# Kernel optimization log

Hardware: AMD Instinct MI355X
Metric: run time of the kernel (lower is better)

Reference implementation:

```python
import jax, jax.numpy as jnp
import numpy as np

B, T, C = 8, 2048, 1024
E, K = 8, 2
CF = 1.0
LB_W = 0.01
H = 4 * C
N = B * T
CAP = max(int(N * K / E * CF), 1)  # 4096
NEG_INF = -1e30


def setup_inputs() -> dict:
    key = jax.random.key(0)
    ks = jax.random.split(key, 10)
    s_r = (2.0 / (C + E)) ** 0.5  # xavier_normal for router linears
    s1 = 1.0 / np.sqrt(C)
    s2 = 1.0 / np.sqrt(H)
    return {
        "x": jax.random.normal(ks[0], (B, T, C), jnp.float32),
        "noise": jax.random.normal(ks[1], (B, T, E), jnp.float32),
        "w_route": jax.random.normal(ks[2], (E, C), jnp.float32) * s_r,
        "b_route": jnp.zeros((E,), jnp.float32),
        "w_noise": jax.random.normal(ks[3], (E, C), jnp.float32) * s_r,
        "b_noise": jnp.zeros((E,), jnp.float32),
        "w1": jax.random.uniform(ks[4], (E, C, H), jnp.float32, -s1, s1),
        "b1": jax.random.uniform(ks[5], (E, H), jnp.float32, -s1, s1),
        "w2": jax.random.uniform(ks[6], (E, H, C), jnp.float32, -s2, s2),
        "b2": jax.random.uniform(ks[7], (E, C), jnp.float32, -s2, s2),
    }


def reference(x, noise, w_route, b_route, w_noise, b_noise, w1, b1, w2, b2):
    # ---- NoisyTopkRouter ----
    logits = jnp.einsum('btc,ec->bte', x, w_route) + b_route          # (B,T,E)
    noise_std = jax.nn.softplus(jnp.einsum('btc,ec->bte', x, w_noise) + b_noise)
    noisy = logits + noise * noise_std
    topk_vals, topk_idx = jax.lax.top_k(noisy, K)                     # (B,T,K)
    # sparse softmax: -inf everywhere except top-k slots
    onehot = jax.nn.one_hot(topk_idx, E, dtype=noisy.dtype)           # (B,T,K,E)
    sel = onehot.max(axis=-2) > 0                                     # (B,T,E) bool
    gates = jax.nn.softmax(jnp.where(sel, noisy, NEG_INF), axis=-1)   # (B,T,E)

    # ---- load balancing loss ----
    frac = gates.mean(axis=(0, 1))
    lb_loss = jnp.mean((frac - 1.0 / E) ** 2)

    # ---- capacity-limited dispatch (faithful: first-come order, cap per expert) ----
    gates_f = gates.reshape(N, E)
    mask_f = sel.reshape(N, E)
    pos = jnp.cumsum(mask_f.astype(jnp.int32), axis=0) - 1            # rank within expert
    keep = mask_f & (pos < CAP)
    tok = jnp.broadcast_to(jnp.arange(N, dtype=jnp.int32)[:, None], (N, E))
    eid = jnp.broadcast_to(jnp.arange(E, dtype=jnp.int32)[None, :], (N, E))
    slot = jnp.where(keep, pos, CAP)                                  # CAP = out of bounds -> dropped
    dispatch = jnp.full((E, CAP), N, dtype=jnp.int32)
    dispatch = dispatch.at[eid.ravel(), slot.ravel()].set(tok.ravel(), mode='drop')

    # ---- gather -> per-expert MLP -> weighted scatter ----
    x_pad = jnp.concatenate([x.reshape(N, C), jnp.zeros((1, C), x.dtype)], axis=0)
    xe = x_pad[dispatch]                                              # (E,CAP,C)
    h = jax.nn.relu(jnp.einsum('etc,ech->eth', xe, w1) + b1[:, None, :])
    ye = jnp.einsum('eth,ehc->etc', h, w2) + b2[:, None, :]           # (E,CAP,C)
    g_pad = jnp.concatenate([gates_f, jnp.zeros((1, E), gates_f.dtype)], axis=0)
    g = g_pad[dispatch, jnp.arange(E, dtype=jnp.int32)[:, None]]      # (E,CAP)
    weighted = ye * g[..., None]

    out = jnp.zeros((N + 1, C), x.dtype).at[dispatch.ravel()].add(
        weighted.reshape(E * CAP, C))[:N].reshape(B, T, C)
    return out, LB_W * lb_loss
```

## Files before the change

kernel.cpp:

```cpp
#include <hip/hip_runtime.h>

#define N_TOK 16384
#define C_DIM 1024
#define E_NUM 8
#define H_DIM 4096
#define CAPACITY 4096
#define LB_W 0.01f

typedef __bf16 bf16;
typedef bf16 bf16x8 __attribute__((ext_vector_type(8)));
typedef bf16 bf16x4 __attribute__((ext_vector_type(4)));
typedef float f32x4 __attribute__((ext_vector_type(4)));

__device__ __forceinline__ void gld_lds16(const void* g, void* l) {
  __builtin_amdgcn_global_load_lds((const __attribute__((address_space(1))) void*)g,
                                   (__attribute__((address_space(3))) void*)l,
                                   16, 0, 0);
}

__global__ void route_kernel(const float* __restrict__ x,
                             const float* __restrict__ noise,
                             const float* __restrict__ w_route,
                             const float* __restrict__ b_route,
                             const float* __restrict__ w_noise,
                             const float* __restrict__ b_noise,
                             float* __restrict__ gates,
                             int* __restrict__ maskT) {
  const int lane = threadIdx.x;
  const int n = blockIdx.x * blockDim.y + threadIdx.y;
  float xv[16];
#pragma unroll
  for (int i = 0; i < 16; ++i) xv[i] = x[(size_t)n * C_DIM + lane + 64 * i];
  float lr[E_NUM], ln[E_NUM];
#pragma unroll
  for (int e = 0; e < E_NUM; ++e) {
    float sr = 0.f, sn = 0.f;
#pragma unroll
    for (int i = 0; i < 16; ++i) {
      sr += xv[i] * w_route[e * C_DIM + lane + 64 * i];
      sn += xv[i] * w_noise[e * C_DIM + lane + 64 * i];
    }
#pragma unroll
    for (int off = 32; off; off >>= 1) {
      sr += __shfl_xor(sr, off, 64);
      sn += __shfl_xor(sn, off, 64);
    }
    lr[e] = sr;
    ln[e] = sn;
  }
  if (lane == 0) {
    float noisy[E_NUM];
#pragma unroll
    for (int e = 0; e < E_NUM; ++e) {
      float z = ln[e] + b_noise[e];
      float sp = fmaxf(z, 0.f) + log1pf(expf(-fabsf(z)));
      noisy[e] = lr[e] + b_route[e] + noise[n * E_NUM + e] * sp;
    }
    int i1 = 0;
    float v1 = noisy[0];
#pragma unroll
    for (int e = 1; e < E_NUM; ++e)
      if (noisy[e] > v1) { v1 = noisy[e]; i1 = e; }
    int i2 = -1;
    float v2 = -3.0e38f;
#pragma unroll
    for (int e = 0; e < E_NUM; ++e)
      if (e != i1 && noisy[e] > v2) { v2 = noisy[e]; i2 = e; }
    float e2 = expf(v2 - v1);
    float denom = 1.f + e2;
#pragma unroll
    for (int e = 0; e < E_NUM; ++e) {
      float g = (e == i1) ? (1.f / denom) : ((e == i2) ? (e2 / denom) : 0.f);
      gates[n * E_NUM + e] = g;
      maskT[(size_t)e * N_TOK + n] = (e == i1 || e == i2) ? 1 : 0;
    }
  }
}

__global__ __launch_bounds__(1024) void scan_kernel(
    const int* __restrict__ maskT, const float* __restrict__ gates,
    int* __restrict__ tok, float* __restrict__ gslot) {
  const int e = blockIdx.x;
  const int t = threadIdx.x;
  const int lane = t & 63, w = t >> 6;
  __shared__ int wt[16];

  int4 mv[4];
#pragma unroll
  for (int i = 0; i < 4; ++i)
    mv[i] = *(const int4*)(maskT + (size_t)e * N_TOK + t * 16 + i * 4);
  const int* m = (const int*)mv;
  int s = 0;
#pragma unroll
  for (int i = 0; i < 16; ++i) s += m[i];

  int v = s;
#pragma unroll
  for (int off = 1; off < 64; off <<= 1) {
    int u = __shfl_up(v, off, 64);
    if (lane >= off) v += u;
  }
  if (lane == 63) wt[w] = v;
  __syncthreads();
  int woff = 0;
#pragma unroll
  for (int i = 0; i < 16; ++i)
    if (i < w) woff += wt[i];

  int pos = woff + v - s;
#pragma unroll
  for (int i = 0; i < 16; ++i) {
    if (m[i] && pos < CAPACITY) {
      int n = t * 16 + i;
      tok[e * CAPACITY + pos] = n;
      gslot[e * CAPACITY + pos] = gates[n * E_NUM + e];
    }
    pos += m[i];
  }
}

__global__ void frac_kernel(const float* __restrict__ gates,
                            float* __restrict__ fracsum) {
  __shared__ float sm[E_NUM];
  int t = threadIdx.x;
  if (t < E_NUM) sm[t] = 0.f;
  __syncthreads();
  int g0 = blockIdx.x * 256 + t;
  float p = 0.f;
#pragma unroll
  for (int i = 0; i < (N_TOK * E_NUM) / (256 * 64); ++i)
    p += gates[g0 + i * 256 * 64];
  atomicAdd(&sm[t & 7], p);
  __syncthreads();
  if (t < E_NUM) atomicAdd(&fracsum[t], sm[t]);
}

__global__ void lb_kernel(const float* __restrict__ fracsum,
                          float* __restrict__ out_scalar) {
  if (threadIdx.x == 0) {
    float s = 0.f;
#pragma unroll
    for (int e = 0; e < E_NUM; ++e) {
      float f = fracsum[e] / (float)N_TOK - 0.125f;
      s += f * f;
    }
    out_scalar[0] = LB_W * (s / (float)E_NUM);
  }
}

__global__ void transpose_cvt(const float* __restrict__ src,
                              bf16* __restrict__ dst, int R, int S) {
  __shared__ float tile[32][33];
  const int e = blockIdx.z;
  const int r0 = blockIdx.y * 32;
  const int s0 = blockIdx.x * 32;
  const int t = threadIdx.x;
  const int rr = t >> 3, cc = (t & 7) * 4;
  const float4 v = *(const float4*)(src + ((size_t)e * R + (r0 + rr)) * S + s0 + cc);
  tile[rr][cc + 0] = v.x;
  tile[rr][cc + 1] = v.y;
  tile[rr][cc + 2] = v.z;
  tile[rr][cc + 3] = v.w;
  __syncthreads();
  bf16x4 o;
#pragma unroll
  for (int i = 0; i < 4; ++i) o[i] = (bf16)tile[cc + i][rr];
  *(bf16x4*)(dst + ((size_t)e * S + (s0 + rr)) * R + r0 + cc) = o;
}

__global__ void gather_xe(const float* __restrict__ x,
                          const int* __restrict__ tok, bf16* __restrict__ xe) {
  const int row = blockIdx.x;
  const int t = tok[row];
  const int c = threadIdx.x * 8;
  bf16x8 v;
  if (t >= 0) {
    const float4* xp = (const float4*)(x + (size_t)t * C_DIM + c);
    float4 a = xp[0], b = xp[1];
    v[0] = (bf16)a.x; v[1] = (bf16)a.y; v[2] = (bf16)a.z; v[3] = (bf16)a.w;
    v[4] = (bf16)b.x; v[5] = (bf16)b.y; v[6] = (bf16)b.z; v[7] = (bf16)b.w;
  } else {
#pragma unroll
    for (int i = 0; i < 8; ++i) v[i] = (bf16)0.f;
  }
  *(bf16x8*)(xe + (size_t)row * C_DIM + c) = v;
}

template <int EPI>
__global__ __launch_bounds__(256) void gemm_bt(
    const bf16* __restrict__ A0, size_t aStride, const bf16* __restrict__ B0,
    size_t bStride, int Kk, int Nn, const float* __restrict__ bias0,
    int biasStride, bf16* __restrict__ Hout0, size_t hStride,
    const int* __restrict__ tok0, const float* __restrict__ gslot0,
    float* __restrict__ Out) {
  const int z = blockIdx.z;
  const bf16* A = A0 + (size_t)z * aStride;
  const bf16* B = B0 + (size_t)z * bStride;
  const float* bias = bias0 + (size_t)z * biasStride;

  __shared__ bf16 As[128 * 32];
  __shared__ bf16 Bs[128 * 32];
  const int t = threadIdx.x;
  const int lane = t & 63;
  const int w = t >> 6;
  const int wm = (w >> 1) * 64;
  const int wn = (w & 1) * 64;
  const int bm = blockIdx.y * 128;
  const int bn = blockIdx.x * 128;

  f32x4 acc[4][4] = {};

  const int rowA = t >> 2;
  const int partA = (t & 3) << 4;
  const char* aP1 = (const char*)(A + (size_t)(bm + rowA) * Kk) + partA;
  const char* aP2 = (const char*)(A + (size_t)(bm + 64 + rowA) * Kk) + partA;
  const char* bP1 = (const char*)(B + (size_t)(bn + rowA) * Kk) + partA;
  const char* bP2 = (const char*)(B + (size_t)(bn + 64 + rowA) * Kk) + partA;
  char* asD1 = (char*)As + (t & 192) * 16;
  char* asD2 = (char*)As + 4096 + (t & 192) * 16;
  char* bsD1 = (char*)Bs + (t & 192) * 16;
  char* bsD2 = (char*)Bs + 4096 + (t & 192) * 16;

  for (int kt = 0; kt < Kk; kt += 32) {
    gld_lds16(aP1 + kt * 2, asD1);
    gld_lds16(aP2 + kt * 2, asD2);
    gld_lds16(bP1 + kt * 2, bsD1);
    gld_lds16(bP2 + kt * 2, bsD2);
    __syncthreads();
    bf16x8 af[4], bfr[4];
#pragma unroll
    for (int i = 0; i < 4; ++i) {
      af[i] = *(const bf16x8*)(As + (wm + i * 16 + (lane & 15)) * 32 + (lane >> 4) * 8);
      bfr[i] = *(const bf16x8*)(Bs + (wn + i * 16 + (lane & 15)) * 32 + (lane >> 4) * 8);
    }
#pragma unroll
    for (int i = 0; i < 4; ++i)
#pragma unroll
      for (int j = 0; j < 4; ++j)
        acc[i][j] = __builtin_amdgcn_mfma_f32_16x16x32_bf16(af[i], bfr[j], acc[i][j], 0, 0, 0);
    __syncthreads();
  }

  if (EPI == 0) {
    bf16* Hout = Hout0 + (size_t)z * hStride;
#pragma unroll
    for (int i = 0; i < 4; ++i) {
      const int rbase = bm + wm + i * 16 + (lane >> 4) * 4;
#pragma unroll
      for (int j = 0; j < 4; ++j) {
        const int col = bn + wn + j * 16 + (lane & 15);
        const float b = bias[col];
#pragma unroll
        for (int r = 0; r < 4; ++r) {
          float v = acc[i][j][r] + b;
          Hout[(size_t)(rbase + r) * Nn + col] = (bf16)fmaxf(v, 0.f);
        }
      }
    }
  } else {
    const int* tok = tok0 + (size_t)z * CAPACITY;
    const float* gslot = gslot0 + (size_t)z * CAPACITY;
#pragma unroll
    for (int i = 0; i < 4; ++i) {
      const int rbase = bm + wm + i * 16 + (lane >> 4) * 4;
#pragma unroll
      for (int r = 0; r < 4; ++r) {
        const int row = rbase + r;
        const int tk = tok[row];
        if (tk >= 0) {
          const float g = gslot[row];
#pragma unroll
          for (int j = 0; j < 4; ++j) {
            const int col = bn + wn + j * 16 + (lane & 15);
            atomicAdd(Out + (size_t)tk * C_DIM + col, g * (acc[i][j][r] + bias[col]));
          }
        }
      }
    }
  }
}

extern "C" void kernel_launch(void* const* d_in, const int* in_sizes, int n_in,
                              void* d_out, int out_size, void* d_ws,
                              size_t ws_size, hipStream_t stream) {
  const float* x = (const float*)d_in[0];
  const float* noise = (const float*)d_in[1];
  const float* w_route = (const float*)d_in[2];
  const float* b_route = (const float*)d_in[3];
  const float* w_noise = (const float*)d_in[4];
  const float* b_noise = (const float*)d_in[5];
  const float* w1 = (const float*)d_in[6];
  const float* b1 = (const float*)d_in[7];
  const float* w2 = (const float*)d_in[8];
  const float* b2 = (const float*)d_in[9];
  float* out = (float*)d_out;

  char* ws = (char*)d_ws;
  size_t off = 0;
  auto alloc = [&](size_t bytes) {
    char* p = ws + off;
    off += (bytes + 255) & ~(size_t)255;
    return p;
  };
  float* gates = (float*)alloc((size_t)N_TOK * E_NUM * 4);
  int* maskT = (int*)alloc((size_t)N_TOK * E_NUM * 4);
  int* tok = (int*)alloc((size_t)E_NUM * CAPACITY * 4);
  float* gslot = (float*)alloc((size_t)E_NUM * CAPACITY * 4);
  float* fracsum = (float*)alloc(256);
  bf16* xe = (bf16*)alloc((size_t)E_NUM * CAPACITY * C_DIM * 2);
  bf16* w1t = (bf16*)alloc((size_t)E_NUM * H_DIM * C_DIM * 2);
  bf16* w2t = (bf16*)alloc((size_t)E_NUM * C_DIM * H_DIM * 2);

  const size_t hPer = (size_t)CAPACITY * H_DIM * 2;
  size_t hAvail = (ws_size > off) ? (ws_size - off) : 0;
  int G = (int)(hAvail / hPer);
  if (G > E_NUM) G = E_NUM;
  if (G < 1) return;
  while (E_NUM % G) --G;
  bf16* hbuf = (bf16*)alloc((size_t)G * hPer);

  hipMemsetAsync(d_out, 0, (size_t)out_size * 4, stream);
  hipMemsetAsync(tok, 0xFF, (size_t)E_NUM * CAPACITY * 4, stream);
  hipMemsetAsync(fracsum, 0, 256, stream);

  transpose_cvt<<<dim3(H_DIM / 32, C_DIM / 32, E_NUM), 256, 0, stream>>>(w1, w1t, C_DIM, H_DIM);
  transpose_cvt<<<dim3(C_DIM / 32, H_DIM / 32, E_NUM), 256, 0, stream>>>(w2, w2t, H_DIM, C_DIM);

  route_kernel<<<dim3(N_TOK / 4), dim3(64, 4), 0, stream>>>(
      x, noise, w_route, b_route, w_noise, b_noise, gates, maskT);
  scan_kernel<<<E_NUM, 1024, 0, stream>>>(maskT, gates, tok, gslot);
  frac_kernel<<<64, 256, 0, stream>>>(gates, fracsum);
  lb_kernel<<<1, 64, 0, stream>>>(fracsum, out + (size_t)N_TOK * C_DIM);

  gather_xe<<<E_NUM * CAPACITY, 128, 0, stream>>>(x, tok, xe);

  for (int e0 = 0; e0 < E_NUM; e0 += G) {
    gemm_bt<0><<<dim3(H_DIM / 128, CAPACITY / 128, G), 256, 0, stream>>>(
        xe + (size_t)e0 * CAPACITY * C_DIM, (size_t)CAPACITY * C_DIM,
        w1t + (size_t)e0 * H_DIM * C_DIM, (size_t)H_DIM * C_DIM,
        C_DIM, H_DIM, b1 + (size_t)e0 * H_DIM, H_DIM,
        hbuf, (size_t)CAPACITY * H_DIM, nullptr, nullptr, nullptr);
    gemm_bt<1><<<dim3(C_DIM / 128, CAPACITY / 128, G), 256, 0, stream>>>(
        hbuf, (size_t)CAPACITY * H_DIM,
        w2t + (size_t)e0 * C_DIM * H_DIM, (size_t)C_DIM * H_DIM,
        H_DIM, C_DIM, b2 + (size_t)e0 * C_DIM, C_DIM,
        nullptr, 0, tok + (size_t)e0 * CAPACITY, gslot + (size_t)e0 * CAPACITY, out);
  }
}
```

Baseline: 1.499 ms.

## Merge gates and mask into transposed buffer; remap GEMM block order across XCDs

```diff
diff --git a/kernel.cpp b/kernel.cpp
--- a/kernel.cpp
+++ b/kernel.cpp
@@ -24,8 +24,7 @@
                              const float* __restrict__ b_route,
                              const float* __restrict__ w_noise,
                              const float* __restrict__ b_noise,
-                             float* __restrict__ gates,
-                             int* __restrict__ maskT) {
+                             float* __restrict__ gatesT) {
   const int lane = threadIdx.x;
   const int n = blockIdx.x * blockDim.y + threadIdx.y;
   float xv[16];
@@ -70,29 +69,32 @@
     float denom = 1.f + e2;
 #pragma unroll
     for (int e = 0; e < E_NUM; ++e) {
-      float g = (e == i1) ? (1.f / denom) : ((e == i2) ? (e2 / denom) : 0.f);
-      gates[n * E_NUM + e] = g;
-      maskT[(size_t)e * N_TOK + n] = (e == i1 || e == i2) ? 1 : 0;
+      float g = (e == i1) ? (1.f / denom) : ((e == i2) ? (e2 / denom) : -1.f);
+      gatesT[(size_t)e * N_TOK + n] = g;
     }
   }
 }
 
 __global__ __launch_bounds__(1024) void scan_kernel(
-    const int* __restrict__ maskT, const float* __restrict__ gates,
-    int* __restrict__ tok, float* __restrict__ gslot) {
+    const float* __restrict__ gatesT, int* __restrict__ tok,
+    float* __restrict__ gslot) {
   const int e = blockIdx.x;
   const int t = threadIdx.x;
   const int lane = t & 63, w = t >> 6;
   __shared__ int wt[16];
 
-  int4 mv[4];
+  float4 gv[4];
 #pragma unroll
   for (int i = 0; i < 4; ++i)
-    mv[i] = *(const int4*)(maskT + (size_t)e * N_TOK + t * 16 + i * 4);
-  const int* m = (const int*)mv;
+    gv[i] = *(const float4*)(gatesT + (size_t)e * N_TOK + t * 16 + i * 4);
+  const float* g = (const float*)gv;
+  int m[16];
   int s = 0;
 #pragma unroll
-  for (int i = 0; i < 16; ++i) s += m[i];
+  for (int i = 0; i < 16; ++i) {
+    m[i] = (g[i] >= 0.f) ? 1 : 0;
+    s += m[i];
+  }
 
   int v = s;
 #pragma unroll
@@ -111,28 +113,30 @@
 #pragma unroll
   for (int i = 0; i < 16; ++i) {
     if (m[i] && pos < CAPACITY) {
-      int n = t * 16 + i;
-      tok[e * CAPACITY + pos] = n;
-      gslot[e * CAPACITY + pos] = gates[n * E_NUM + e];
+      tok[e * CAPACITY + pos] = t * 16 + i;
+      gslot[e * CAPACITY + pos] = g[i];
     }
     pos += m[i];
   }
 }
 
-__global__ void frac_kernel(const float* __restrict__ gates,
+__global__ void frac_kernel(const float* __restrict__ gatesT,
                             float* __restrict__ fracsum) {
-  __shared__ float sm[E_NUM];
-  int t = threadIdx.x;
-  if (t < E_NUM) sm[t] = 0.f;
+  __shared__ float red[256];
+  const int e = blockIdx.x, t = threadIdx.x;
+  float s = 0.f;
+#pragma unroll
+  for (int i = 0; i < 16; ++i) {
+    float4 v = *(const float4*)(gatesT + (size_t)e * N_TOK + (i * 256 + t) * 4);
+    s += fmaxf(v.x, 0.f) + fmaxf(v.y, 0.f) + fmaxf(v.z, 0.f) + fmaxf(v.w, 0.f);
+  }
+  red[t] = s;
   __syncthreads();
-  int g0 = blockIdx.x * 256 + t;
-  float p = 0.f;
-#pragma unroll
-  for (int i = 0; i < (N_TOK * E_NUM) / (256 * 64); ++i)
-    p += gates[g0 + i * 256 * 64];
-  atomicAdd(&sm[t & 7], p);
-  __syncthreads();
-  if (t < E_NUM) atomicAdd(&fracsum[t], sm[t]);
+  for (int off = 128; off; off >>= 1) {
+    if (t < off) red[t] += red[t + off];
+    __syncthreads();
+  }
+  if (t == 0) fracsum[e] = red[0];
 }
 
 __global__ void lb_kernel(const float* __restrict__ fracsum,
@@ -198,6 +202,12 @@
   const bf16* B = B0 + (size_t)z * bStride;
   const float* bias = bias0 + (size_t)z * biasStride;
 
+  const int nbid = blockIdx.y * gridDim.x + blockIdx.x;
+  const int per = (gridDim.x * gridDim.y) >> 3;
+  const int lin = (nbid & 7) * per + (nbid >> 3);
+  const int bm = (lin / gridDim.x) * 128;
+  const int bn = (lin % gridDim.x) * 128;
+
   __shared__ bf16 As[128 * 32];
   __shared__ bf16 Bs[128 * 32];
   const int t = threadIdx.x;
@@ -205,8 +215,6 @@
   const int w = t >> 6;
   const int wm = (w >> 1) * 64;
   const int wn = (w & 1) * 64;
-  const int bm = blockIdx.y * 128;
-  const int bn = blockIdx.x * 128;
 
   f32x4 acc[4][4] = {};
 
@@ -302,8 +310,7 @@
     off += (bytes + 255) & ~(size_t)255;
     return p;
   };
-  float* gates = (float*)alloc((size_t)N_TOK * E_NUM * 4);
-  int* maskT = (int*)alloc((size_t)N_TOK * E_NUM * 4);
+  float* gatesT = (float*)alloc((size_t)N_TOK * E_NUM * 4);
   int* tok = (int*)alloc((size_t)E_NUM * CAPACITY * 4);
   float* gslot = (float*)alloc((size_t)E_NUM * CAPACITY * 4);
   float* fracsum = (float*)alloc(256);
@@ -321,15 +328,14 @@
 
   hipMemsetAsync(d_out, 0, (size_t)out_size * 4, stream);
   hipMemsetAsync(tok, 0xFF, (size_t)E_NUM * CAPACITY * 4, stream);
-  hipMemsetAsync(fracsum, 0, 256, stream);
 
   transpose_cvt<<<dim3(H_DIM / 32, C_DIM / 32, E_NUM), 256, 0, stream>>>(w1, w1t, C_DIM, H_DIM);
   transpose_cvt<<<dim3(C_DIM / 32, H_DIM / 32, E_NUM), 256, 0, stream>>>(w2, w2t, H_DIM, C_DIM);
 
   route_kernel<<<dim3(N_TOK / 4), dim3(64, 4), 0, stream>>>(
-      x, noise, w_route, b_route, w_noise, b_noise, gates, maskT);
-  scan_kernel<<<E_NUM, 1024, 0, stream>>>(maskT, gates, tok, gslot);
-  frac_kernel<<<64, 256, 0, stream>>>(gates, fracsum);
+      x, noise, w_route, b_route, w_noise, b_noise, gatesT);
+  scan_kernel<<<E_NUM, 1024, 0, stream>>>(gatesT, tok, gslot);
+  frac_kernel<<<E_NUM, 256, 0, stream>>>(gatesT, fracsum);
   lb_kernel<<<1, 64, 0, stream>>>(fracsum, out + (size_t)N_TOK * C_DIM);
 
   gather_xe<<<E_NUM * CAPACITY, 128, 0, stream>>>(x, tok, xe);
```

New measurement: 1.468 ms. 1.02x faster.
